# Performance work log

Hardware: AMD Instinct MI355X
Metric: run time of the kernel (lower is better)

## Reference

```python
import jax, jax.numpy as jnp
import numpy as np

N, D, DIN, S, R = 128, 2560, 5120, 16, 160  # users, d_model, d_inner, d_state, dt_rank


def setup_inputs() -> dict:
    key = jax.random.key(0)
    ks = jax.random.split(key, 16)
    f = lambda k, shape, s: jax.random.normal(k, shape, dtype=jnp.float32) * s
    return {
        "x": f(ks[0], (1, 1, N, D), 1.0),
        "conv_state0": f(ks[1], (1, 1, N, DIN), 0.1),
        "conv_state1": f(ks[2], (1, 1, N, DIN), 0.1),
        "conv_state2": f(ks[3], (1, 1, N, DIN), 0.1),
        "conv_state3": f(ks[4], (1, 1, N, DIN), 0.1),
        "ssm_state": f(ks[5], (N, DIN, S), 0.1),
        "ssm_proj": f(ks[6], (D, DIN), 0.02),
        "mlp_proj": f(ks[7], (D, DIN), 0.02),
        "down_proj": f(ks[8], (DIN, D), 0.02),
        "conv_w": f(ks[9], (4, DIN), 0.2),
        "conv_bias": f(ks[10], (DIN,), 0.1),
        "x_proj_w": f(ks[11], (DIN, R + 2 * S), 0.02),
        "dt_proj_w": f(ks[12], (R, DIN), 0.05),
        "dt_proj_b": f(ks[13], (DIN,), 0.1),
        "A_log": jnp.log(jnp.broadcast_to(jnp.arange(1, S + 1, dtype=jnp.float32), (DIN, S))),
        "D_param": jnp.ones((DIN,), jnp.float32),
    }


def reference(x, conv_state0, conv_state1, conv_state2, conv_state3, ssm_state,
              ssm_proj, mlp_proj, down_proj, conv_w, conv_bias,
              x_proj_w, dt_proj_w, dt_proj_b, A_log, D_param):
    r = dt_proj_w.shape[0]
    s = A_log.shape[1]
    x2 = x[0, 0]                         # (N, D)
    xs = x2 @ ssm_proj                   # (N, DIN) in_proj (ssm half)
    # shifted conv state window: oldest state (conv_state0) is dropped
    states = (conv_state1[0, 0], conv_state2[0, 0], conv_state3[0, 0], xs)
    conv_out = conv_bias + conv_w[0] * states[0] + conv_w[1] * states[1] \
        + conv_w[2] * states[2] + conv_w[3] * states[3]   # (N, DIN)
    u = jax.nn.silu(conv_out)
    # selective-scan single step (TtMambaSSM)
    proj = u @ x_proj_w                  # (N, R + 2S)
    dt = jax.nn.softplus(proj[:, :r] @ dt_proj_w + dt_proj_b)  # (N, DIN)
    Bm = proj[:, r:r + s]                # (N, S)
    Cm = proj[:, r + s:]                 # (N, S)
    A = -jnp.exp(A_log)                  # (DIN, S)
    dA = jnp.exp(dt[:, :, None] * A[None])                     # (N, DIN, S)
    h = dA * ssm_state + dt[:, :, None] * Bm[:, None, :] * u[:, :, None]
    y = jnp.einsum('nds,ns->nd', h, Cm) + D_param * u          # (N, DIN)
    # residual/gate branch and output projection (note: no silu on res, as in source)
    res = x2 @ mlp_proj                  # (N, DIN)
    out = (y * res) @ down_proj          # (N, D)
    return out[None, None]               # (1, 1, N, D)
```

## Files before the change

kernel.cpp:

```cpp
#include <hip/hip_runtime.h>

using u16 = unsigned short;
using u32 = unsigned int;

typedef __attribute__((ext_vector_type(8))) short short8;
typedef __attribute__((ext_vector_type(4))) float floatx4;

constexpr int TOKENS = 128;
constexpr int DM = 2560;
constexpr int DI = 5120;
constexpr int NS = 16;
constexpr int NR = 160;
constexpr int NP = 192;

constexpr size_t XS_OFF   = 0;
constexpr size_t RES_OFF  = XS_OFF  + (size_t)TOKENS * DI;
constexpr size_t U_OFF    = RES_OFF + (size_t)TOKENS * DI;
constexpr size_t DT_OFF   = U_OFF   + (size_t)TOKENS * DI;
constexpr size_t PROJ_OFF = DT_OFF  + (size_t)TOKENS * DI;
constexpr size_t OACC_OFF = PROJ_OFF + (size_t)TOKENS * NP;

__device__ __forceinline__ float bf2f(u16 h) {
  u32 u = ((u32)h) << 16;
  return __builtin_bit_cast(float, u);
}
__device__ __forceinline__ u16 f2bf(float f) {
  u32 u = __builtin_bit_cast(u32, f);
  u += 0x7FFFu + ((u >> 16) & 1u);
  return (u16)(u >> 16);
}
__device__ __forceinline__ u32 pk2(float a, float b) {
  return (u32)f2bf(a) | ((u32)f2bf(b) << 16);
}
__device__ __forceinline__ float ldsc(const void* p, size_t i, bool bf) {
  return bf ? bf2f(((const u16*)p)[i]) : ((const float*)p)[i];
}
__device__ __forceinline__ uint4 ld8(const void* p, size_t i, bool bf) {
  if (bf) return *(const uint4*)((const u16*)p + i);
  const float4* f = (const float4*)((const float*)p + i);
  float4 a = f[0], b = f[1];
  return (uint4){pk2(a.x, a.y), pk2(a.z, a.w), pk2(b.x, b.y), pk2(b.z, b.w)};
}

struct GemmP {
  const void* A; int lda; int a_ws;
  const void* B; const void* B2;
  float* C; float* C2;
  int ldb; int ldc;
  int ksteps;
  int nx_half;
  const u32* probe;
};

__global__ __launch_bounds__(256, 4) void gemm_k(GemmP p) {
  __shared__ u16 As[128 * 40];
  __shared__ u16 Bs[32 * 64];

  const bool bf = (p.probe[0] != 0u);
  const int tid = threadIdx.x;
  const int bx = blockIdx.x;
  const void* B = p.B; float* C = p.C;
  int nblk = bx;
  if (bx >= p.nx_half) { B = p.B2; C = p.C2; nblk = bx - p.nx_half; }
  const int n0 = nblk * 64;
  const int kstart = blockIdx.y * p.ksteps * 32;

  const int wave = tid >> 6, lane = tid & 63;
  const int q = lane >> 4, l16 = lane & 15;
  const int wx = wave & 1, wy = wave >> 1;

  const bool a_f32 = p.a_ws || !bf;
  const int am = (tid + 0) >> 2, asg = tid & 3;
  const int am2 = (tid + 256) >> 2;
  const int bk = tid >> 3, bsg = tid & 7;

  floatx4 acc[4][2];
#pragma unroll
  for (int mi = 0; mi < 4; mi++)
#pragma unroll
    for (int ni = 0; ni < 2; ni++) acc[mi][ni] = (floatx4){0.f, 0.f, 0.f, 0.f};

  uint4 aW[2], bW;
  auto load_tiles = [&](int ks, uint4* aO, uint4& bO) {
    const int kbase = kstart + ks * 32;
    if (!a_f32) {
      aO[0] = *(const uint4*)((const u16*)p.A + (size_t)am * p.lda + kbase + asg * 8);
      aO[1] = *(const uint4*)((const u16*)p.A + (size_t)am2 * p.lda + kbase + asg * 8);
    } else {
      const float4* f0 = (const float4*)((const float*)p.A + (size_t)am * p.lda + kbase + asg * 8);
      const float4* f1 = (const float4*)((const float*)p.A + (size_t)am2 * p.lda + kbase + asg * 8);
      float4 a0 = f0[0], a1 = f0[1], b0 = f1[0], b1 = f1[1];
      aO[0] = (uint4){pk2(a0.x, a0.y), pk2(a0.z, a0.w), pk2(a1.x, a1.y), pk2(a1.z, a1.w)};
      aO[1] = (uint4){pk2(b0.x, b0.y), pk2(b0.z, b0.w), pk2(b1.x, b1.y), pk2(b1.z, b1.w)};
    }
    bO = ld8(B, (size_t)(kbase + bk) * p.ldb + n0 + bsg * 8, bf);
  };

  load_tiles(0, aW, bW);

  for (int ks = 0;;) {
    __syncthreads();
    *(uint4*)&As[am * 40 + asg * 8] = aW[0];
    *(uint4*)&As[am2 * 40 + asg * 8] = aW[1];
    {
      int off = ((bsg << 4) + ((bk >> 3) << 5)) & 127;
      *(uint4*)&Bs[bk * 64 + (off >> 1)] = bW;
    }
    __syncthreads();

    uint4 aN[2], bN;
    const bool more = (ks + 1 < p.ksteps);
    if (more) load_tiles(ks + 1, aN, bN);

    short8 afr[4];
#pragma unroll
    for (int mi = 0; mi < 4; mi++)
      afr[mi] = __builtin_bit_cast(short8,
          *(const uint4*)&As[(wy * 64 + mi * 16 + l16) * 40 + q * 8]);
    short8 bfr[2];
#pragma unroll
    for (int ni = 0; ni < 2; ni++) {
      int nl2 = (wx * 32 + ni * 16 + l16) * 2;
      int boff = (nl2 + (q << 5)) & 127;
      const u16* bp = &Bs[q * 512 + (boff >> 1)];
      short8 b;
#pragma unroll
      for (int j = 0; j < 8; j++) b[j] = (short)bp[j * 64];
      bfr[ni] = b;
    }
#pragma unroll
    for (int mi = 0; mi < 4; mi++)
#pragma unroll
      for (int ni = 0; ni < 2; ni++)
        acc[mi][ni] = __builtin_amdgcn_mfma_f32_16x16x32_bf16(
            afr[mi], bfr[ni], acc[mi][ni], 0, 0, 0);

    if (!more) break;
    aW[0] = aN[0]; aW[1] = aN[1]; bW = bN;
    ks++;
  }

#pragma unroll
  for (int ni = 0; ni < 2; ni++) {
    int col = n0 + wx * 32 + ni * 16 + l16;
#pragma unroll
    for (int mi = 0; mi < 4; mi++) {
      floatx4 v = acc[mi][ni];
#pragma unroll
      for (int r = 0; r < 4; r++) {
        int row = wy * 64 + mi * 16 + q * 4 + r;
        atomicAdd(&C[(size_t)row * p.ldc + col], v[r]);
      }
    }
  }
}

__global__ __launch_bounds__(256) void epi_u_k(
    const float* __restrict__ xs_acc, const void* __restrict__ cs1,
    const void* __restrict__ cs2, const void* __restrict__ cs3,
    const void* __restrict__ cw, const void* __restrict__ cb,
    float* __restrict__ u, const u32* __restrict__ probe) {
  const bool bf = (probe[0] != 0u);
  const int n = blockIdx.y;
  const int d = blockIdx.x * 256 + threadIdx.x;
  const size_t nd = (size_t)n * DI + d;
  float cv = ldsc(cb, d, bf) + ldsc(cw, d, bf) * ldsc(cs1, nd, bf) +
             ldsc(cw, DI + d, bf) * ldsc(cs2, nd, bf) +
             ldsc(cw, 2 * DI + d, bf) * ldsc(cs3, nd, bf) +
             ldsc(cw, 3 * DI + d, bf) * xs_acc[nd];
  u[nd] = cv / (1.0f + __expf(-cv));
}

__global__ __launch_bounds__(256) void ssm_k(
    const void* __restrict__ sstate, const void* __restrict__ alog,
    const void* __restrict__ dparam, const void* __restrict__ dtb,
    const float* __restrict__ proj, const float* __restrict__ dtacc,
    const float* __restrict__ u, const float* __restrict__ res,
    float* __restrict__ z, const u32* __restrict__ probe) {
  const bool bf = (probe[0] != 0u);
  const int n = blockIdx.y;
  const int d = blockIdx.x * 256 + threadIdx.x;
  __shared__ float Bsh[NS], Csh[NS];
  if (threadIdx.x < NS)
    Bsh[threadIdx.x] = proj[(size_t)n * NP + NR + threadIdx.x];
  else if (threadIdx.x < 2 * NS)
    Csh[threadIdx.x - NS] = proj[(size_t)n * NP + NR + threadIdx.x];
  __syncthreads();
  const size_t nd = (size_t)n * DI + d;
  const float uv = u[nd], rv = res[nd];
  float sv = dtacc[nd] + ldsc(dtb, d, bf);
  const float dtv = (sv > 20.0f) ? sv : log1pf(__expf(sv));

  float stf[16], alf[16];
  if (bf) {
    u16 st[16], al[16];
    const uint4* sp = (const uint4*)((const u16*)sstate + nd * 16);
    *(uint4*)&st[0] = sp[0]; *(uint4*)&st[8] = sp[1];
    const uint4* ap = (const uint4*)((const u16*)alog + (size_t)d * 16);
    *(uint4*)&al[0] = ap[0]; *(uint4*)&al[8] = ap[1];
#pragma unroll
    for (int s = 0; s < 16; s++) { stf[s] = bf2f(st[s]); alf[s] = bf2f(al[s]); }
  } else {
    const float4* sp = (const float4*)((const float*)sstate + nd * 16);
    const float4* ap = (const float4*)((const float*)alog + (size_t)d * 16);
#pragma unroll
    for (int i = 0; i < 4; i++) {
      float4 s4 = sp[i], a4 = ap[i];
      stf[i * 4 + 0] = s4.x; stf[i * 4 + 1] = s4.y; stf[i * 4 + 2] = s4.z; stf[i * 4 + 3] = s4.w;
      alf[i * 4 + 0] = a4.x; alf[i * 4 + 1] = a4.y; alf[i * 4 + 2] = a4.z; alf[i * 4 + 3] = a4.w;
    }
  }
  float y = 0.f;
#pragma unroll
  for (int s = 0; s < 16; s++) {
    float Aa = -__expf(alf[s]);
    float dA = __expf(dtv * Aa);
    float h = dA * stf[s] + dtv * Bsh[s] * uv;
    y += h * Csh[s];
  }
  y += ldsc(dparam, d, bf) * uv;
  z[nd] = y * rv;
}

__global__ __launch_bounds__(256) void cvt_k(const float* __restrict__ in,
                                             void* __restrict__ out, int n,
                                             const u32* __restrict__ probe) {
  const bool bf = (probe[0] != 0u);
  int i = blockIdx.x * 256 + threadIdx.x;
  if (i < n) {
    if (bf) ((u16*)out)[i] = f2bf(in[i]);
    else    ((float*)out)[i] = in[i];
  }
}

extern "C" void kernel_launch(void* const* d_in, const int* in_sizes, int n_in,
                              void* d_out, int out_size, void* d_ws, size_t ws_size,
                              hipStream_t stream) {
  const void* x         = d_in[0];
  const void* cs1       = d_in[2];
  const void* cs2       = d_in[3];
  const void* cs3       = d_in[4];
  const void* ssm_state = d_in[5];
  const void* ssm_proj  = d_in[6];
  const void* mlp_proj  = d_in[7];
  const void* down_proj = d_in[8];
  const void* conv_w    = d_in[9];
  const void* conv_b    = d_in[10];
  const void* x_proj_w  = d_in[11];
  const void* dt_proj_w = d_in[12];
  const void* dt_proj_b = d_in[13];
  const void* A_log     = d_in[14];
  const void* D_param   = d_in[15];
  const u32*  probe     = (const u32*)A_log;

  float* ws     = (float*)d_ws;
  float* xs_acc = ws + XS_OFF;
  float* z      = ws + XS_OFF;
  float* res    = ws + RES_OFF;
  float* u      = ws + U_OFF;
  float* dtacc  = ws + DT_OFF;
  float* proj   = ws + PROJ_OFF;
  float* oacc   = ws + OACC_OFF;

  hipMemsetAsync(xs_acc, 0, (size_t)TOKENS * DI * sizeof(float), stream);
  hipMemsetAsync(res,    0, (size_t)TOKENS * DI * sizeof(float), stream);
  hipMemsetAsync(dtacc,  0, (size_t)TOKENS * DI * sizeof(float), stream);
  hipMemsetAsync(proj,   0, (size_t)TOKENS * NP * sizeof(float), stream);
  hipMemsetAsync(oacc,   0, (size_t)TOKENS * DM * sizeof(float), stream);

  {
    GemmP p{};
    p.A = x; p.lda = DM; p.a_ws = 0;
    p.B = ssm_proj; p.B2 = mlp_proj;
    p.C = xs_acc; p.C2 = res;
    p.ldb = DI; p.ldc = DI;
    p.ksteps = DM / 32 / 8; p.nx_half = 80;
    p.probe = probe;
    gemm_k<<<dim3(160, 8), 256, 0, stream>>>(p);
  }
  epi_u_k<<<dim3(DI / 256, TOKENS), 256, 0, stream>>>(
      xs_acc, cs1, cs2, cs3, conv_w, conv_b, u, probe);
  {
    GemmP p{};
    p.A = u; p.lda = DI; p.a_ws = 1;
    p.B = x_proj_w; p.B2 = nullptr;
    p.C = proj; p.C2 = nullptr;
    p.ldb = NP; p.ldc = NP;
    p.ksteps = 4; p.nx_half = 1 << 30;
    p.probe = probe;
    gemm_k<<<dim3(3, 40), 256, 0, stream>>>(p);
  }
  {
    GemmP p{};
    p.A = proj; p.lda = NP; p.a_ws = 1;
    p.B = dt_proj_w; p.B2 = nullptr;
    p.C = dtacc; p.C2 = nullptr;
    p.ldb = DI; p.ldc = DI;
    p.ksteps = 1; p.nx_half = 1 << 30;
    p.probe = probe;
    gemm_k<<<dim3(DI / 64, 5), 256, 0, stream>>>(p);
  }
  ssm_k<<<dim3(DI / 256, TOKENS), 256, 0, stream>>>(
      ssm_state, A_log, D_param, dt_proj_b, proj, dtacc, u, res, z, probe);
  {
    GemmP p{};
    p.A = z; p.lda = DI; p.a_ws = 1;
    p.B = down_proj; p.B2 = nullptr;
    p.C = oacc; p.C2 = nullptr;
    p.ldb = DM; p.ldc = DM;
    p.ksteps = DI / 32 / 16; p.nx_half = 1 << 30;
    p.probe = probe;
    gemm_k<<<dim3(DM / 64, 16), 256, 0, stream>>>(p);
  }
  cvt_k<<<dim3((out_size + 255) / 256), 256, 0, stream>>>(oacc, d_out, out_size, probe);
}
```

Before: 321.7 us.

## Replace atomic split-K with partial-sum buffers and bf16 intermediate activations

Each GEMM now writes its split-K partials to a workspace arena with plain stores, and small reduction kernels sum them, replacing the fp32 atomicAdd accumulation and the five memsets. Intermediates (x, u, res, z, proj) are stored as bf16, so GEMM A-loads need no fp32-to-bf16 packing and move half the bytes. The N tile shrinks to 32 columns to keep grids wide. The cost is extra partial-buffer traffic and reduction launches, plus extra rounding of res and u to bf16.

```diff
diff --git a/kernel.cpp b/kernel.cpp
--- a/kernel.cpp
+++ b/kernel.cpp
@@ -12,13 +12,20 @@
 constexpr int NS = 16;
 constexpr int NR = 160;
 constexpr int NP = 192;
-
-constexpr size_t XS_OFF   = 0;
-constexpr size_t RES_OFF  = XS_OFF  + (size_t)TOKENS * DI;
-constexpr size_t U_OFF    = RES_OFF + (size_t)TOKENS * DI;
-constexpr size_t DT_OFF   = U_OFF   + (size_t)TOKENS * DI;
-constexpr size_t PROJ_OFF = DT_OFF  + (size_t)TOKENS * DI;
-constexpr size_t OACC_OFF = PROJ_OFF + (size_t)TOKENS * NP;
+constexpr int NWIDE = DI * 2;
+
+constexpr size_t ARENA_OFF = 0;
+constexpr size_t ARENA_SZ  = 2 * (size_t)TOKENS * NWIDE;
+constexpr size_t P1_OFF    = ARENA_OFF;
+constexpr size_t P3_OFF    = ARENA_OFF;
+constexpr size_t DT_OFF    = ARENA_OFF + 10 * (size_t)TOKENS * NP;
+constexpr size_t P6_OFF    = ARENA_OFF;
+constexpr size_t XBF_OFF   = ARENA_OFF + ARENA_SZ;
+constexpr size_t UBF_OFF   = XBF_OFF + (size_t)TOKENS * DM / 2;
+constexpr size_t RESBF_OFF = UBF_OFF + (size_t)TOKENS * DI / 2;
+constexpr size_t ZBF_OFF   = RESBF_OFF + (size_t)TOKENS * DI / 2;
+constexpr size_t PROJ_OFF  = ZBF_OFF + (size_t)TOKENS * DI / 2;
+constexpr size_t PABF_OFF  = PROJ_OFF + (size_t)TOKENS * NP;
 
 __device__ __forceinline__ float bf2f(u16 h) {
   u32 u = ((u32)h) << 16;
@@ -35,17 +42,16 @@
 __device__ __forceinline__ float ldsc(const void* p, size_t i, bool bf) {
   return bf ? bf2f(((const u16*)p)[i]) : ((const float*)p)[i];
 }
-__device__ __forceinline__ uint4 ld8(const void* p, size_t i, bool bf) {
-  if (bf) return *(const uint4*)((const u16*)p + i);
-  const float4* f = (const float4*)((const float*)p + i);
-  float4 a = f[0], b = f[1];
-  return (uint4){pk2(a.x, a.y), pk2(a.z, a.w), pk2(b.x, b.y), pk2(b.z, b.w)};
+__device__ __forceinline__ uint2 ld4pk(const void* p, size_t i, bool bf) {
+  if (bf) return *(const uint2*)((const u16*)p + i);
+  const float4 f = *(const float4*)((const float*)p + i);
+  return (uint2){pk2(f.x, f.y), pk2(f.z, f.w)};
 }
 
 struct GemmP {
-  const void* A; int lda; int a_ws;
+  const u16* A; int lda;
   const void* B; const void* B2;
-  float* C; float* C2;
+  float* C;
   int ldb; int ldc;
   int ksteps;
   int nx_half;
@@ -54,46 +60,36 @@
 
 __global__ __launch_bounds__(256, 4) void gemm_k(GemmP p) {
   __shared__ u16 As[128 * 40];
-  __shared__ u16 Bs[32 * 64];
+  __shared__ u16 Bs[32 * 34 + 6];
 
   const bool bf = (p.probe[0] != 0u);
   const int tid = threadIdx.x;
   const int bx = blockIdx.x;
-  const void* B = p.B; float* C = p.C;
-  int nblk = bx;
-  if (bx >= p.nx_half) { B = p.B2; C = p.C2; nblk = bx - p.nx_half; }
-  const int n0 = nblk * 64;
+  const int colbase = bx * 32;
+  const void* B = p.B;
+  int bn0 = colbase;
+  if (bx >= p.nx_half) { B = p.B2; bn0 = colbase - p.nx_half * 32; }
+  float* C = p.C + (size_t)blockIdx.y * 128 * p.ldc;
   const int kstart = blockIdx.y * p.ksteps * 32;
 
   const int wave = tid >> 6, lane = tid & 63;
   const int q = lane >> 4, l16 = lane & 15;
   const int wx = wave & 1, wy = wave >> 1;
 
-  const bool a_f32 = p.a_ws || !bf;
-  const int am = (tid + 0) >> 2, asg = tid & 3;
+  const int am = tid >> 2, asg = tid & 3;
   const int am2 = (tid + 256) >> 2;
   const int bk = tid >> 3, bsg = tid & 7;
 
-  floatx4 acc[4][2];
-#pragma unroll
-  for (int mi = 0; mi < 4; mi++)
-#pragma unroll
-    for (int ni = 0; ni < 2; ni++) acc[mi][ni] = (floatx4){0.f, 0.f, 0.f, 0.f};
-
-  uint4 aW[2], bW;
-  auto load_tiles = [&](int ks, uint4* aO, uint4& bO) {
+  floatx4 acc[4];
+#pragma unroll
+  for (int mi = 0; mi < 4; mi++) acc[mi] = (floatx4){0.f, 0.f, 0.f, 0.f};
+
+  uint4 aW[2]; uint2 bW;
+  auto load_tiles = [&](int ks, uint4* aO, uint2& bO) {
     const int kbase = kstart + ks * 32;
-    if (!a_f32) {
-      aO[0] = *(const uint4*)((const u16*)p.A + (size_t)am * p.lda + kbase + asg * 8);
-      aO[1] = *(const uint4*)((const u16*)p.A + (size_t)am2 * p.lda + kbase + asg * 8);
-    } else {
-      const float4* f0 = (const float4*)((const float*)p.A + (size_t)am * p.lda + kbase + asg * 8);
-      const float4* f1 = (const float4*)((const float*)p.A + (size_t)am2 * p.lda + kbase + asg * 8);
-      float4 a0 = f0[0], a1 = f0[1], b0 = f1[0], b1 = f1[1];
-      aO[0] = (uint4){pk2(a0.x, a0.y), pk2(a0.z, a0.w), pk2(a1.x, a1.y), pk2(a1.z, a1.w)};
-      aO[1] = (uint4){pk2(b0.x, b0.y), pk2(b0.z, b0.w), pk2(b1.x, b1.y), pk2(b1.z, b1.w)};
-    }
-    bO = ld8(B, (size_t)(kbase + bk) * p.ldb + n0 + bsg * 8, bf);
+    aO[0] = *(const uint4*)(p.A + (size_t)am * p.lda + kbase + asg * 8);
+    aO[1] = *(const uint4*)(p.A + (size_t)am2 * p.lda + kbase + asg * 8);
+    bO = ld4pk(B, (size_t)(kbase + bk) * p.ldb + bn0 + bsg * 4, bf);
   };
 
   load_tiles(0, aW, bW);
@@ -103,12 +99,12 @@
     *(uint4*)&As[am * 40 + asg * 8] = aW[0];
     *(uint4*)&As[am2 * 40 + asg * 8] = aW[1];
     {
-      int off = ((bsg << 4) + ((bk >> 3) << 5)) & 127;
-      *(uint4*)&Bs[bk * 64 + (off >> 1)] = bW;
+      u32* bd = (u32*)&Bs[bk * 34 + bsg * 4];
+      bd[0] = bW.x; bd[1] = bW.y;
     }
     __syncthreads();
 
-    uint4 aN[2], bN;
+    uint4 aN[2]; uint2 bN;
     const bool more = (ks + 1 < p.ksteps);
     if (more) load_tiles(ks + 1, aN, bN);
 
@@ -117,66 +113,84 @@
     for (int mi = 0; mi < 4; mi++)
       afr[mi] = __builtin_bit_cast(short8,
           *(const uint4*)&As[(wy * 64 + mi * 16 + l16) * 40 + q * 8]);
-    short8 bfr[2];
-#pragma unroll
-    for (int ni = 0; ni < 2; ni++) {
-      int nl2 = (wx * 32 + ni * 16 + l16) * 2;
-      int boff = (nl2 + (q << 5)) & 127;
-      const u16* bp = &Bs[q * 512 + (boff >> 1)];
+    short8 bfr;
+    {
+      const int nloc = wx * 16 + l16;
+      const u16* bp = &Bs[q * 272 + nloc];
       short8 b;
 #pragma unroll
-      for (int j = 0; j < 8; j++) b[j] = (short)bp[j * 64];
-      bfr[ni] = b;
+      for (int j = 0; j < 8; j++) b[j] = (short)bp[j * 34];
+      bfr = b;
     }
 #pragma unroll
     for (int mi = 0; mi < 4; mi++)
-#pragma unroll
-      for (int ni = 0; ni < 2; ni++)
-        acc[mi][ni] = __builtin_amdgcn_mfma_f32_16x16x32_bf16(
-            afr[mi], bfr[ni], acc[mi][ni], 0, 0, 0);
+      acc[mi] = __builtin_amdgcn_mfma_f32_16x16x32_bf16(afr[mi], bfr, acc[mi], 0, 0, 0);
 
     if (!more) break;
     aW[0] = aN[0]; aW[1] = aN[1]; bW = bN;
     ks++;
   }
 
-#pragma unroll
-  for (int ni = 0; ni < 2; ni++) {
-    int col = n0 + wx * 32 + ni * 16 + l16;
-#pragma unroll
-    for (int mi = 0; mi < 4; mi++) {
-      floatx4 v = acc[mi][ni];
-#pragma unroll
-      for (int r = 0; r < 4; r++) {
-        int row = wy * 64 + mi * 16 + q * 4 + r;
-        atomicAdd(&C[(size_t)row * p.ldc + col], v[r]);
-      }
+  const int col = colbase + wx * 16 + l16;
+#pragma unroll
+  for (int mi = 0; mi < 4; mi++) {
+#pragma unroll
+    for (int r = 0; r < 4; r++) {
+      int row = wy * 64 + mi * 16 + q * 4 + r;
+      C[(size_t)row * p.ldc + col] = acc[mi][r];
     }
   }
 }
 
-__global__ __launch_bounds__(256) void epi_u_k(
-    const float* __restrict__ xs_acc, const void* __restrict__ cs1,
+__global__ __launch_bounds__(256) void cvta_k(const void* __restrict__ x,
+                                              u16* __restrict__ xbf, int n,
+                                              const u32* __restrict__ probe) {
+  const bool bf = (probe[0] != 0u);
+  int i = blockIdx.x * 256 + threadIdx.x;
+  if (i < n) xbf[i] = bf ? ((const u16*)x)[i] : f2bf(((const float*)x)[i]);
+}
+
+__global__ __launch_bounds__(256) void r1_k(
+    const float* __restrict__ P1, const void* __restrict__ cs1,
     const void* __restrict__ cs2, const void* __restrict__ cs3,
     const void* __restrict__ cw, const void* __restrict__ cb,
-    float* __restrict__ u, const u32* __restrict__ probe) {
+    u16* __restrict__ ubf, u16* __restrict__ resbf,
+    const u32* __restrict__ probe) {
   const bool bf = (probe[0] != 0u);
   const int n = blockIdx.y;
-  const int d = blockIdx.x * 256 + threadIdx.x;
-  const size_t nd = (size_t)n * DI + d;
-  float cv = ldsc(cb, d, bf) + ldsc(cw, d, bf) * ldsc(cs1, nd, bf) +
-             ldsc(cw, DI + d, bf) * ldsc(cs2, nd, bf) +
-             ldsc(cw, 2 * DI + d, bf) * ldsc(cs3, nd, bf) +
-             ldsc(cw, 3 * DI + d, bf) * xs_acc[nd];
-  u[nd] = cv / (1.0f + __expf(-cv));
+  const int c = blockIdx.x * 256 + threadIdx.x;
+  const size_t idx = (size_t)n * NWIDE + c;
+  float v = P1[idx] + P1[(size_t)TOKENS * NWIDE + idx];
+  if (c < DI) {
+    const size_t nd = (size_t)n * DI + c;
+    float cv = ldsc(cb, c, bf) + ldsc(cw, c, bf) * ldsc(cs1, nd, bf) +
+               ldsc(cw, DI + c, bf) * ldsc(cs2, nd, bf) +
+               ldsc(cw, 2 * DI + c, bf) * ldsc(cs3, nd, bf) +
+               ldsc(cw, 3 * DI + c, bf) * v;
+    float uu = cv / (1.0f + __expf(-cv));
+    ubf[nd] = f2bf(uu);
+  } else {
+    resbf[(size_t)n * DI + (c - DI)] = f2bf(v);
+  }
+}
+
+__global__ __launch_bounds__(256) void r3_k(const float* __restrict__ P3,
+                                            float* __restrict__ proj,
+                                            u16* __restrict__ pabf) {
+  int i = blockIdx.x * 256 + threadIdx.x;
+  float s = 0.f;
+#pragma unroll
+  for (int p = 0; p < 10; p++) s += P3[(size_t)p * TOKENS * NP + i];
+  proj[i] = s;
+  pabf[i] = f2bf(s);
 }
 
 __global__ __launch_bounds__(256) void ssm_k(
     const void* __restrict__ sstate, const void* __restrict__ alog,
     const void* __restrict__ dparam, const void* __restrict__ dtb,
     const float* __restrict__ proj, const float* __restrict__ dtacc,
-    const float* __restrict__ u, const float* __restrict__ res,
-    float* __restrict__ z, const u32* __restrict__ probe) {
+    const u16* __restrict__ ubf, const u16* __restrict__ resbf,
+    u16* __restrict__ zbf, const u32* __restrict__ probe) {
   const bool bf = (probe[0] != 0u);
   const int n = blockIdx.y;
   const int d = blockIdx.x * 256 + threadIdx.x;
@@ -187,7 +201,7 @@
     Csh[threadIdx.x - NS] = proj[(size_t)n * NP + NR + threadIdx.x];
   __syncthreads();
   const size_t nd = (size_t)n * DI + d;
-  const float uv = u[nd], rv = res[nd];
+  const float uv = bf2f(ubf[nd]), rv = bf2f(resbf[nd]);
   float sv = dtacc[nd] + ldsc(dtb, d, bf);
   const float dtv = (sv > 20.0f) ? sv : log1pf(__expf(sv));
 
@@ -219,18 +233,20 @@
     y += h * Csh[s];
   }
   y += ldsc(dparam, d, bf) * uv;
-  z[nd] = y * rv;
-}
-
-__global__ __launch_bounds__(256) void cvt_k(const float* __restrict__ in,
-                                             void* __restrict__ out, int n,
-                                             const u32* __restrict__ probe) {
+  zbf[nd] = f2bf(y * rv);
+}
+
+__global__ __launch_bounds__(256) void r6_k(const float* __restrict__ P6,
+                                            void* __restrict__ out, int n,
+                                            const u32* __restrict__ probe) {
   const bool bf = (probe[0] != 0u);
   int i = blockIdx.x * 256 + threadIdx.x;
-  if (i < n) {
-    if (bf) ((u16*)out)[i] = f2bf(in[i]);
-    else    ((float*)out)[i] = in[i];
-  }
+  if (i >= n) return;
+  float s = 0.f;
+#pragma unroll
+  for (int p = 0; p < 8; p++) s += P6[(size_t)p * TOKENS * DM + i];
+  if (bf) ((u16*)out)[i] = f2bf(s);
+  else    ((float*)out)[i] = s;
 }
 
 extern "C" void kernel_launch(void* const* d_in, const int* in_sizes, int n_in,
@@ -253,64 +269,60 @@
   const void* D_param   = d_in[15];
   const u32*  probe     = (const u32*)A_log;
 
-  float* ws     = (float*)d_ws;
-  float* xs_acc = ws + XS_OFF;
-  float* z      = ws + XS_OFF;
-  float* res    = ws + RES_OFF;
-  float* u      = ws + U_OFF;
-  float* dtacc  = ws + DT_OFF;
-  float* proj   = ws + PROJ_OFF;
-  float* oacc   = ws + OACC_OFF;
-
-  hipMemsetAsync(xs_acc, 0, (size_t)TOKENS * DI * sizeof(float), stream);
-  hipMemsetAsync(res,    0, (size_t)TOKENS * DI * sizeof(float), stream);
-  hipMemsetAsync(dtacc,  0, (size_t)TOKENS * DI * sizeof(float), stream);
-  hipMemsetAsync(proj,   0, (size_t)TOKENS * NP * sizeof(float), stream);
-  hipMemsetAsync(oacc,   0, (size_t)TOKENS * DM * sizeof(float), stream);
+  float* ws    = (float*)d_ws;
+  float* P1    = ws + P1_OFF;
+  float* P3    = ws + P3_OFF;
+  float* dtacc = ws + DT_OFF;
+  float* P6    = ws + P6_OFF;
+  u16*   xbf   = (u16*)(ws + XBF_OFF);
+  u16*   ubf   = (u16*)(ws + UBF_OFF);
+  u16*   resbf = (u16*)(ws + RESBF_OFF);
+  u16*   zbf   = (u16*)(ws + ZBF_OFF);
+  float* proj  = ws + PROJ_OFF;
+  u16*   pabf  = (u16*)(ws + PABF_OFF);
+
+  cvta_k<<<dim3((TOKENS * DM + 255) / 256), 256, 0, stream>>>(x, xbf, TOKENS * DM, probe);
 
   {
     GemmP p{};
-    p.A = x; p.lda = DM; p.a_ws = 0;
+    p.A = xbf; p.lda = DM;
     p.B = ssm_proj; p.B2 = mlp_proj;
-    p.C = xs_acc; p.C2 = res;
-    p.ldb = DI; p.ldc = DI;
-    p.ksteps = DM / 32 / 8; p.nx_half = 80;
+    p.C = P1; p.ldb = DI; p.ldc = NWIDE;
+    p.ksteps = DM / 32 / 2; p.nx_half = DI / 32;
     p.probe = probe;
-    gemm_k<<<dim3(160, 8), 256, 0, stream>>>(p);
-  }
-  epi_u_k<<<dim3(DI / 256, TOKENS), 256, 0, stream>>>(
-      xs_acc, cs1, cs2, cs3, conv_w, conv_b, u, probe);
+    gemm_k<<<dim3(NWIDE / 32, 2), 256, 0, stream>>>(p);
+  }
+  r1_k<<<dim3(NWIDE / 256, TOKENS), 256, 0, stream>>>(
+      P1, cs1, cs2, cs3, conv_w, conv_b, ubf, resbf, probe);
   {
     GemmP p{};
-    p.A = u; p.lda = DI; p.a_ws = 1;
+    p.A = ubf; p.lda = DI;
     p.B = x_proj_w; p.B2 = nullptr;
-    p.C = proj; p.C2 = nullptr;
-    p.ldb = NP; p.ldc = NP;
-    p.ksteps = 4; p.nx_half = 1 << 30;
+    p.C = P3; p.ldb = NP; p.ldc = NP;
+    p.ksteps = DI / 32 / 10; p.nx_half = 1 << 30;
     p.probe = probe;
-    gemm_k<<<dim3(3, 40), 256, 0, stream>>>(p);
-  }
+    gemm_k<<<dim3(NP / 32, 10), 256, 0, stream>>>(p);
+  }
+  r3_k<<<dim3(TOKENS * NP / 256), 256, 0, stream>>>(P3, proj, pabf);
   {
     GemmP p{};
-    p.A = proj; p.lda = NP; p.a_ws = 1;
+    p.A = pabf; p.lda = NP;
     p.B = dt_proj_w; p.B2 = nullptr;
-    p.C = dtacc; p.C2 = nullptr;
-    p.ldb = DI; p.ldc = DI;
-    p.ksteps = 1; p.nx_half = 1 << 30;
+    p.C = dtacc; p.ldb = DI; p.ldc = DI;
+    p.ksteps = NR / 32; p.nx_half = 1 << 30;
     p.probe = probe;
-    gemm_k<<<dim3(DI / 64, 5), 256, 0, stream>>>(p);
+    gemm_k<<<dim3(DI / 32, 1), 256, 0, stream>>>(p);
   }
   ssm_k<<<dim3(DI / 256, TOKENS), 256, 0, stream>>>(
-      ssm_state, A_log, D_param, dt_proj_b, proj, dtacc, u, res, z, probe);
+      ssm_state, A_log, D_param, dt_proj_b, proj, dtacc, ubf, resbf, zbf, probe);
   {
     GemmP p{};
-    p.A = z; p.lda = DI; p.a_ws = 1;
+    p.A = zbf; p.lda = DI;
     p.B = down_proj; p.B2 = nullptr;
-    p.C = oacc; p.C2 = nullptr;
-    p.ldb = DM; p.ldc = DM;
-    p.ksteps = DI / 32 / 16; p.nx_half = 1 << 30;
+    p.C = P6; p.ldb = DM; p.ldc = DM;
+    p.ksteps = DI / 32 / 8; p.nx_half = 1 << 30;
     p.probe = probe;
-    gemm_k<<<dim3(DM / 64, 16), 256, 0, stream>>>(p);
-  }
-  cvt_k<<<dim3((out_size + 255) / 256), 256, 0, stream>>>(oacc, d_out, out_size, probe);
-}
+    gemm_k<<<dim3(DM / 32, 8), 256, 0, stream>>>(p);
+  }
+  r6_k<<<dim3((out_size + 255) / 256), 256, 0, stream>>>(P6, d_out, out_size, probe);
+}
```

New measurement: 472.4 us. 1.47x slower.
